# Optimization experiments

Hardware: AMD Instinct MI355X
Metric: run time of the kernel (lower is better)

The kernel has to match this reference:

```python
import jax, jax.numpy as jnp
import numpy as np


def _conv1x1(x, w, b):
    # x: [B,C,H,W], w: [O,C], b: [O] -> [B,O,H,W]
    return jnp.einsum('bchw,oc->bohw', x, w) + b[None, :, None, None]


def _maxpool2x2(x):
    # MaxPool2d(kernel_size=2, stride=2), VALID padding
    return jax.lax.reduce_window(
        x, -jnp.inf, jax.lax.max,
        window_dimensions=(1, 1, 2, 2),
        window_strides=(1, 1, 2, 2),
        padding='VALID')


def setup_inputs() -> dict:
    key = jax.random.key(0)
    ks = jax.random.split(key, 9)
    B, C, H, W = 8, 256, 64, 64
    c = 128  # in_channels // channel_scale_factor
    s = 0.05
    return {
        'x': jax.random.normal(ks[0], (B, C, H, W), jnp.float32),
        'theta_w': jax.random.normal(ks[1], (c, C), jnp.float32) * s,
        'theta_b': jax.random.normal(ks[2], (c,), jnp.float32) * s,
        'phi_w': jax.random.normal(ks[3], (c, C), jnp.float32) * s,
        'phi_b': jax.random.normal(ks[4], (c,), jnp.float32) * s,
        'g_w': jax.random.normal(ks[5], (c, C), jnp.float32) * s,
        'g_b': jax.random.normal(ks[6], (c,), jnp.float32) * s,
        'wz_w': jax.random.normal(ks[7], (C, c), jnp.float32) * s,
        'wz_b': jax.random.normal(ks[8], (C,), jnp.float32) * s,
    }


def reference(x, theta_w, theta_b, phi_w, phi_b, g_w, g_b, wz_w, wz_b):
    B, C, H, W = x.shape
    c = theta_w.shape[0]
    ox = x
    theta = _conv1x1(x, theta_w, theta_b)              # [B,c,H,W]
    xp = _maxpool2x2(x)                                # [B,C,h,w]
    phi = _conv1x1(xp, phi_w, phi_b)                   # [B,c,h,w]
    gi = _conv1x1(xp, g_w, g_b)                        # [B,c,h,w]

    N = H * W
    M = phi.shape[2] * phi.shape[3]
    theta1 = theta.reshape(B, c, N).transpose(0, 2, 1)  # [B,N,c]
    phi1 = phi.reshape(B, c, M)                         # [B,c,M]
    gi1 = gi.reshape(B, c, M).transpose(0, 2, 1)        # [B,M,c]

    m1 = jnp.einsum('bnc,bcm->bnm', theta1, phi1)       # [B,N,M] attention scores
    m1 = jax.nn.softmax(m1, axis=2)
    m2 = jnp.einsum('bnm,bmc->bnc', m1, gi1)            # [B,N,c]
    # Faithful to torch .view: raw-buffer reinterpretation, no transpose
    m3 = m2.reshape(B, c, H, W)
    m4 = _conv1x1(m3, wz_w, wz_b)                       # [B,C,H,W]
    return m4 + ox
```

## Files before the change

### kernel.cpp

```cpp
#include <hip/hip_runtime.h>
#include <math.h>

#define BATCH 8
#define CINCH 256
#define CMID  128
#define NPIX  4096
#define MPIX  1024

typedef __attribute__((ext_vector_type(8))) short bf16x8;
typedef __attribute__((ext_vector_type(4))) short s16x4;
typedef __attribute__((ext_vector_type(4))) float f32x4;

static __device__ __forceinline__ short f2bf(float f) {
    unsigned u = __float_as_uint(f);
    u = (u + 0x7fffu + ((u >> 16) & 1u)) >> 16;
    return (short)u;
}
static __device__ __forceinline__ float bf2f(short s) {
    return __uint_as_float(((unsigned)(unsigned short)s) << 16);
}

static __device__ __forceinline__ void gl16(const void* g, void* l) {
    __builtin_amdgcn_global_load_lds(
        (const __attribute__((address_space(1))) void*)g,
        (__attribute__((address_space(3))) void*)l, 16, 0, 0);
}

__global__ __launch_bounds__(256)
void wcvt_k(const float* __restrict__ a, const float* __restrict__ b,
            const float* __restrict__ c, const float* __restrict__ d,
            short* __restrict__ o)
{
    int i = (blockIdx.x * 256 + threadIdx.x) * 4;
    if (i < 32768) {
        int cr = i >> 8, col = i & 255;
        int R = (cr & 7) * 16 + (cr >> 3);
        float4 v = *(const float4*)(a + i);
        s16x4 rv = { f2bf(v.x * 1.44269504f), f2bf(v.y * 1.44269504f),
                     f2bf(v.z * 1.44269504f), f2bf(v.w * 1.44269504f) };
        *(s16x4*)(o + R * 256 + col) = rv;
    } else {
        const float* src; int j;
        if (i < 65536)      { src = b; j = i - 32768; }
        else if (i < 98304) { src = c; j = i - 65536; }
        else                { src = d; j = i - 98304; }
        float4 v = *(const float4*)(src + j);
        s16x4 rv = { f2bf(v.x), f2bf(v.y), f2bf(v.z), f2bf(v.w) };
        *(s16x4*)(o + i) = rv;
    }
}

__global__ __launch_bounds__(512)
void front_k(const float* __restrict__ x,
             const short* __restrict__ th_wh, const float* __restrict__ th_b,
             const short* __restrict__ ph_wh, const float* __restrict__ ph_b,
             const short* __restrict__ g_wh,  const float* __restrict__ g_b,
             short* __restrict__ thetaO, short* __restrict__ phiO,
             short* __restrict__ gO)
{
    __shared__ float F[128 * 65];
    __shared__ short X[128 * 264];
    __shared__ short P[32 * 264];

    const int bid = blockIdx.x;
    const int t   = threadIdx.x;
    const int b   = bid & 7;
    const int r   = bid >> 3;
    const int wv  = t >> 6;
    const int l   = t & 63;
    const int lr  = l & 15;
    const int lg  = l >> 4;

    const int hh = wv & 1;
    const int c0 = t >> 7;
    float ra[16], rb[16];
    {
        const float* xb = x + ((size_t)(b * 256)) * 4096 + r * 128;
#pragma unroll
        for (int i = 0; i < 16; ++i)
            ra[i] = xb[(size_t)(c0 + i * 4) * 4096 + hh * 64 + l];
    }
#pragma unroll
    for (int ct = 0; ct < 4; ++ct) {
        if ((ct & 1) == 0) {
#pragma unroll
            for (int i = 0; i < 16; ++i) F[(hh * 64 + l) * 65 + c0 + i * 4] = ra[i];
            if (ct < 3) {
                const float* xb = x + ((size_t)(b * 256 + (ct + 1) * 64)) * 4096 + r * 128;
#pragma unroll
                for (int i = 0; i < 16; ++i)
                    rb[i] = xb[(size_t)(c0 + i * 4) * 4096 + hh * 64 + l];
            }
        } else {
#pragma unroll
            for (int i = 0; i < 16; ++i) F[(hh * 64 + l) * 65 + c0 + i * 4] = rb[i];
            if (ct < 3) {
                const float* xb = x + ((size_t)(b * 256 + (ct + 1) * 64)) * 4096 + r * 128;
#pragma unroll
                for (int i = 0; i < 16; ++i)
                    ra[i] = xb[(size_t)(c0 + i * 4) * 4096 + hh * 64 + l];
            }
        }
        asm volatile("s_waitcnt lgkmcnt(0)" ::: "memory");
        __builtin_amdgcn_s_barrier();
#pragma unroll
        for (int i = 0; i < 16; ++i) {
            int row = wv + i * 8;
            X[row * 264 + ct * 64 + l] = f2bf(F[row * 65 + l]);
        }
        asm volatile("s_waitcnt lgkmcnt(0)" ::: "memory");
        __builtin_amdgcn_s_barrier();
    }

#pragma unroll
    for (int i = 0; i < 4; ++i) {
        int slot = i * 512 + t;
        int wp = slot >> 6, c4 = slot & 63;
        s16x4 v0 = *(const s16x4*)(X + (2 * wp) * 264 + c4 * 4);
        s16x4 v1 = *(const s16x4*)(X + (2 * wp + 1) * 264 + c4 * 4);
        s16x4 v2 = *(const s16x4*)(X + (64 + 2 * wp) * 264 + c4 * 4);
        s16x4 v3 = *(const s16x4*)(X + (65 + 2 * wp) * 264 + c4 * 4);
        s16x4 rm;
#pragma unroll
        for (int e = 0; e < 4; ++e) {
            float m = fmaxf(fmaxf(bf2f(v0[e]), bf2f(v1[e])),
                            fmaxf(bf2f(v2[e]), bf2f(v3[e])));
            rm[e] = f2bf(m);
        }
        *(s16x4*)(P + wp * 264 + c4 * 4) = rm;
    }
    __syncthreads();

    {
        const int m0 = wv * 16;
        f32x4 o[8];
#pragma unroll
        for (int dt = 0; dt < 8; ++dt)
#pragma unroll
            for (int e = 0; e < 4; ++e) o[dt][e] = 0.f;
        for (int kt = 0; kt < 8; ++kt) {
            bf16x8 a = *(const bf16x8*)(X + (m0 + lr) * 264 + kt * 32 + lg * 8);
#pragma unroll
            for (int dt = 0; dt < 8; ++dt) {
                bf16x8 bv = *(const bf16x8*)(th_wh + (size_t)(dt * 16 + lr) * 256 + kt * 32 + lg * 8);
                o[dt] = __builtin_amdgcn_mfma_f32_16x16x32_bf16(a, bv, o[dt], 0, 0, 0);
            }
        }
        float bvt[8];
#pragma unroll
        for (int dt = 0; dt < 8; ++dt) bvt[dt] = th_b[lr * 8 + dt] * 1.44269504f;
        short* ob = thetaO + (size_t)b * NPIX * 128;
#pragma unroll
        for (int rr = 0; rr < 4; ++rr) {
            int n = r * 128 + m0 + lg * 4 + rr;
            bf16x8 sv;
#pragma unroll
            for (int dt = 0; dt < 8; ++dt) sv[dt] = f2bf(o[dt][rr] + bvt[dt]);
            *(bf16x8*)(ob + (size_t)n * 128 + lr * 8) = sv;
        }
    }

    {
        const int half = wv & 1;
        const int coH  = (wv >> 1) & 1;
        const short* wsel = ((wv < 4) ? ph_wh : g_wh) + (size_t)coH * 64 * 256;
        const float* bsel = (wv < 4) ? ph_b : g_b;

        f32x4 q[4];
#pragma unroll
        for (int dt = 0; dt < 4; ++dt)
#pragma unroll
            for (int e = 0; e < 4; ++e) q[dt][e] = 0.f;
        for (int kt = 0; kt < 8; ++kt) {
            bf16x8 a = *(const bf16x8*)(P + (half * 16 + lr) * 264 + kt * 32 + lg * 8);
#pragma unroll
            for (int dt = 0; dt < 4; ++dt) {
                bf16x8 bv = *(const bf16x8*)(wsel + (size_t)(dt * 16 + lr) * 256 + kt * 32 + lg * 8);
                q[dt] = __builtin_amdgcn_mfma_f32_16x16x32_bf16(a, bv, q[dt], 0, 0, 0);
            }
        }
        float bv4[4];
#pragma unroll
        for (int dt = 0; dt < 4; ++dt) bv4[dt] = bsel[coH * 64 + dt * 16 + lr];

        if (wv < 4) {
            short* cb = phiO + (size_t)b * 32 * 4096 + (size_t)r * 4096;
#pragma unroll
            for (int rr = 0; rr < 4; ++rr) {
                int mloc = half * 16 + lg * 4 + rr;
                short* cbb = cb + (mloc >> 4) * 512 + (mloc & 15) * 8;
#pragma unroll
                for (int dt = 0; dt < 4; ++dt) {
                    int cc = coH * 64 + dt * 16 + lr;
                    cbb[(cc >> 5) * 1024 + ((cc >> 3) & 3) * 128 + (cc & 7)]
                        = f2bf(q[dt][rr] + bv4[dt]);
                }
            }
        } else {
            short* cb = gO + (size_t)b * 32 * 4096 + (size_t)r * 4096;
            const int keyblk = half * 2 + (lg >> 1);
#pragma unroll
            for (int dt = 0; dt < 4; ++dt) {
                int cc = coH * 64 + dt * 16 + lr;
                s16x4 sv;
#pragma unroll
                for (int rr = 0; rr < 4; ++rr) sv[rr] = f2bf(q[dt][rr] + bv4[dt]);
                *(s16x4*)(cb + (size_t)((cc >> 4) * 64 + keyblk * 16 + (cc & 15)) * 8
                             + (lg & 1) * 4) = sv;
            }
        }
    }
}

__global__ __launch_bounds__(512)
void attn_fz(const short* __restrict__ theta, const short* __restrict__ phi_sw,
             const short* __restrict__ G_sw, const short* __restrict__ wzh,
             const float* __restrict__ wzb, const float* __restrict__ x,
             float* __restrict__ out)
{
    __shared__ __align__(16) char smem[147456];
    const int t   = threadIdx.x;
    const int wv  = t >> 6;
    const int l   = t & 63;
    const int lr  = l & 15;
    const int lg  = l >> 4;
    const int gid = wv >> 2;
    const int wvl = wv & 3;
    const int bid = blockIdx.x;
    const int b   = bid & 7;
    const int s   = bid >> 3;

    const short* thb = theta + (size_t)b * NPIX * 128;
    const char*  phC = (const char*)phi_sw + (size_t)b * 32 * 8192;
    const char*  gC  = (const char*)G_sw  + (size_t)b * 32 * 8192;
    const int first = gid * 16;

    auto STAGEP = [&](int bufi, int pi) {
#pragma unroll
        for (int sub = 0; sub < 2; ++sub) {
            int chunk = first + pi * 2 + sub;
            const char* ps = phC + (size_t)chunk * 8192 + wvl * 2048 + l * 16;
            const char* gs = gC  + (size_t)chunk * 8192 + wvl * 2048 + l * 16;
            char* base = smem + gid * 65536 + bufi * 32768 + sub * 16384;
            gl16(ps,        base + wvl * 2048);
            gl16(ps + 1024, base + wvl * 2048 + 1024);
            gl16(gs,        base + 8192 + wvl * 2048);
            gl16(gs + 1024, base + 8192 + wvl * 2048 + 1024);
        }
    };

    STAGEP(0, 0);

    bf16x8 bq[2][4];
#pragma unroll
    for (int u = 0; u < 2; ++u) {
        int n = ((wvl * 2 + u) * 16 + lr) * 32 + s;
#pragma unroll
        for (int kt = 0; kt < 4; ++kt)
            bq[u][kt] = *(const bf16x8*)(thb + (size_t)n * 128 + kt * 32 + lg * 8);
    }

    f32x4 o[2][8];
#pragma unroll
    for (int u = 0; u < 2; ++u)
#pragma unroll
        for (int dt = 0; dt < 8; ++dt)
#pragma unroll
            for (int e = 0; e < 4; ++e) o[u][dt][e] = 0.f;
    float ps_[2] = { 0.f, 0.f };

    for (int pi = 0; pi < 8; ++pi) {
        asm volatile("s_waitcnt vmcnt(0)" ::: "memory");
        __builtin_amdgcn_s_barrier();
        if (pi < 7) STAGEP((pi + 1) & 1, pi + 1);

#pragma unroll
        for (int sub = 0; sub < 2; ++sub) {
            const short* pb = (const short*)(smem + gid * 65536 + (pi & 1) * 32768
                                             + sub * 16384);
            const short* gb = pb + 4096;

            f32x4 ssw[2][2];
#pragma unroll
            for (int u = 0; u < 2; ++u)
#pragma unroll
                for (int mt = 0; mt < 2; ++mt)
#pragma unroll
                    for (int e = 0; e < 4; ++e) ssw[u][mt][e] = 0.f;
#pragma unroll
            for (int kt = 0; kt < 4; ++kt) {
                bf16x8 a0 = *(const bf16x8*)(pb + ((kt * 2 + 0) * 64 + l) * 8);
                bf16x8 a1 = *(const bf16x8*)(pb + ((kt * 2 + 1) * 64 + l) * 8);
#pragma unroll
                for (int u = 0; u < 2; ++u) {
                    ssw[u][0] = __builtin_amdgcn_mfma_f32_16x16x32_bf16(a0, bq[u][kt], ssw[u][0], 0, 0, 0);
                    ssw[u][1] = __builtin_amdgcn_mfma_f32_16x16x32_bf16(a1, bq[u][kt], ssw[u][1], 0, 0, 0);
                }
            }

            bf16x8 gf[8];
#pragma unroll
            for (int dt = 0; dt < 8; ++dt)
                gf[dt] = *(const bf16x8*)(gb + (dt * 64 + l) * 8);

#pragma unroll
            for (int u = 0; u < 2; ++u) {
                short* pu = (short*)(smem + 131072 + wv * 2048 + u * 1024);
#pragma unroll
                for (int mt = 0; mt < 2; ++mt) {
                    s16x4 pv;
#pragma unroll
                    for (int rr = 0; rr < 4; ++rr) {
                        float p = exp2f(ssw[u][mt][rr] - 40.f);
                        ps_[u] += p;
                        pv[rr] = f2bf(p);
                    }
                    *(s16x4*)(pu + ((mt * 2 + (lg >> 1)) * 16 + lr) * 8 + (lg & 1) * 4) = pv;
                }
                bf16x8 pa = *(const bf16x8*)(pu + l * 8);
#pragma unroll
                for (int dt = 0; dt < 8; ++dt)
                    o[u][dt] = __builtin_amdgcn_mfma_f32_16x16x32_bf16(pa, gf[dt], o[u][dt], 0, 0, 0);
            }
        }
    }

    __syncthreads();
    float* mg = (float*)smem;
    short* m3l = (short*)(smem + 73728);
    if (wv >= 4) {
        float* mb = mg + (size_t)((wv - 4) * 64 + l) * 68;
#pragma unroll
        for (int u = 0; u < 2; ++u)
#pragma unroll
            for (int dt = 0; dt < 8; ++dt)
                *(f32x4*)(mb + (u * 8 + dt) * 4) = o[u][dt];
        mb[64] = ps_[0]; mb[65] = ps_[1];
    }
    __syncthreads();
    if (wv < 4) {
        const float* mb = mg + (size_t)(wv * 64 + l) * 68;
#pragma unroll
        for (int u = 0; u < 2; ++u)
#pragma unroll
            for (int dt = 0; dt < 8; ++dt) {
                f32x4 pv = *(const f32x4*)(mb + (u * 8 + dt) * 4);
#pragma unroll
                for (int e = 0; e < 4; ++e) o[u][dt][e] += pv[e];
            }
        ps_[0] += mb[64]; ps_[1] += mb[65];

#pragma unroll
        for (int u = 0; u < 2; ++u) {
            float tot = ps_[u];
            tot += __shfl_xor(tot, 16);
            tot += __shfl_xor(tot, 32);
            float inv = 1.f / tot;
            float invg[4];
#pragma unroll
            for (int rr = 0; rr < 4; ++rr) invg[rr] = __shfl(inv, lg * 4 + rr);
            const int cmb = (wvl * 2 + u) * 2 + (lg >> 1);
#pragma unroll
            for (int dt = 0; dt < 8; ++dt) {
                s16x4 zv;
#pragma unroll
                for (int rr = 0; rr < 4; ++rr) zv[rr] = f2bf(o[u][dt][rr] * invg[rr]);
                *(s16x4*)(m3l + (size_t)(cmb * 128 + dt * 16 + lr) * 8 + (lg & 1) * 4) = zv;
            }
        }
    }
    __syncthreads();

    {
        const int co0 = wv * 32;
        bf16x8 afr[2][4];
#pragma unroll
        for (int nt = 0; nt < 2; ++nt) {
            int co = co0 + nt * 16 + lr;
#pragma unroll
            for (int kt = 0; kt < 4; ++kt)
                afr[nt][kt] = *(const bf16x8*)(wzh + (size_t)co * 128 + kt * 32 + lg * 8);
        }
        f32x4 oc[2][8];
#pragma unroll
        for (int nt = 0; nt < 2; ++nt)
#pragma unroll
            for (int dt = 0; dt < 8; ++dt)
#pragma unroll
                for (int e = 0; e < 4; ++e) oc[nt][dt][e] = 0.f;

#pragma unroll
        for (int dt = 0; dt < 8; ++dt) {
#pragma unroll
            for (int kt = 0; kt < 4; ++kt) {
                bf16x8 bz = *(const bf16x8*)(m3l + (size_t)((kt * 4 + lg) * 128 + dt * 16 + lr) * 8);
                oc[0][dt] = __builtin_amdgcn_mfma_f32_16x16x32_bf16(afr[0][kt], bz, oc[0][dt], 0, 0, 0);
                oc[1][dt] = __builtin_amdgcn_mfma_f32_16x16x32_bf16(afr[1][kt], bz, oc[1][dt], 0, 0, 0);
            }
        }

#pragma unroll
        for (int nt = 0; nt < 2; ++nt)
#pragma unroll
            for (int rr = 0; rr < 4; ++rr) {
                int co = co0 + nt * 16 + lg * 4 + rr;
                float bv = wzb[co];
                const float* xb = x + ((size_t)b * 256 + co) * 4096 + s * 128;
                float* ob = out + ((size_t)b * 256 + co) * 4096 + s * 128;
#pragma unroll
                for (int dt = 0; dt < 8; ++dt) {
                    int lp = dt * 16 + lr;
                    ob[lp] = oc[nt][dt][rr] + bv + xb[lp];
                }
            }
    }
}

extern "C" void kernel_launch(void* const* d_in, const int* in_sizes, int n_in,
                              void* d_out, int out_size, void* d_ws, size_t ws_size,
                              hipStream_t stream)
{
    const float* x       = (const float*)d_in[0];
    const float* theta_w = (const float*)d_in[1];
    const float* theta_b = (const float*)d_in[2];
    const float* phi_w   = (const float*)d_in[3];
    const float* phi_b   = (const float*)d_in[4];
    const float* g_w     = (const float*)d_in[5];
    const float* g_b     = (const float*)d_in[6];
    const float* wz_w    = (const float*)d_in[7];
    const float* wz_b    = (const float*)d_in[8];
    float* out = (float*)d_out;

    short* ws      = (short*)d_ws;
    short* theta_h = ws;
    short* phi_h   = theta_h + (size_t)4194304;
    short* G_h     = phi_h + (size_t)1048576;
    short* wh      = G_h  + (size_t)1048576;
    short* th_wh = wh;
    short* ph_wh = wh + 32768;
    short* g_wh  = wh + 65536;
    short* wz_wh = wh + 98304;

    wcvt_k<<<dim3(128), 256, 0, stream>>>(theta_w, phi_w, g_w, wz_w, wh);

    front_k<<<dim3(256), 512, 0, stream>>>(x, th_wh, theta_b, ph_wh, phi_b,
                                           g_wh, g_b, theta_h, phi_h, G_h);

    attn_fz<<<dim3(256), 512, 0, stream>>>(theta_h, phi_h, G_h,
                                           wz_wh, wz_b, x, out);
}
```

Before: 73.32 us.

## Widen front kernel to 1024 threads and prefetch epilogue operands earlier

```diff
diff --git a/kernel.cpp b/kernel.cpp
--- a/kernel.cpp
+++ b/kernel.cpp
@@ -50,7 +50,7 @@
     }
 }
 
-__global__ __launch_bounds__(512)
+__global__ __launch_bounds__(1024)
 void front_k(const float* __restrict__ x,
              const short* __restrict__ th_wh, const float* __restrict__ th_b,
              const short* __restrict__ ph_wh, const float* __restrict__ ph_b,
@@ -72,49 +72,50 @@
     const int lg  = l >> 4;
 
     const int hh = wv & 1;
-    const int c0 = t >> 7;
-    float ra[16], rb[16];
+    const int c0 = wv >> 1;
+    float ra[8], rb[8];
     {
         const float* xb = x + ((size_t)(b * 256)) * 4096 + r * 128;
 #pragma unroll
-        for (int i = 0; i < 16; ++i)
-            ra[i] = xb[(size_t)(c0 + i * 4) * 4096 + hh * 64 + l];
+        for (int i = 0; i < 8; ++i)
+            ra[i] = xb[(size_t)(c0 + i * 8) * 4096 + hh * 64 + l];
     }
 #pragma unroll
     for (int ct = 0; ct < 4; ++ct) {
         if ((ct & 1) == 0) {
 #pragma unroll
-            for (int i = 0; i < 16; ++i) F[(hh * 64 + l) * 65 + c0 + i * 4] = ra[i];
+            for (int i = 0; i < 8; ++i) F[(hh * 64 + l) * 65 + c0 + i * 8] = ra[i];
             if (ct < 3) {
                 const float* xb = x + ((size_t)(b * 256 + (ct + 1) * 64)) * 4096 + r * 128;
 #pragma unroll
-                for (int i = 0; i < 16; ++i)
-                    rb[i] = xb[(size_t)(c0 + i * 4) * 4096 + hh * 64 + l];
+                for (int i = 0; i < 8; ++i)
+                    rb[i] = xb[(size_t)(c0 + i * 8) * 4096 + hh * 64 + l];
             }
         } else {
 #pragma unroll
-            for (int i = 0; i < 16; ++i) F[(hh * 64 + l) * 65 + c0 + i * 4] = rb[i];
+            for (int i = 0; i < 8; ++i) F[(hh * 64 + l) * 65 + c0 + i * 8] = rb[i];
             if (ct < 3) {
                 const float* xb = x + ((size_t)(b * 256 + (ct + 1) * 64)) * 4096 + r * 128;
 #pragma unroll
-                for (int i = 0; i < 16; ++i)
-                    ra[i] = xb[(size_t)(c0 + i * 4) * 4096 + hh * 64 + l];
+                for (int i = 0; i < 8; ++i)
+                    ra[i] = xb[(size_t)(c0 + i * 8) * 4096 + hh * 64 + l];
             }
         }
         asm volatile("s_waitcnt lgkmcnt(0)" ::: "memory");
         __builtin_amdgcn_s_barrier();
 #pragma unroll
-        for (int i = 0; i < 16; ++i) {
-            int row = wv + i * 8;
-            X[row * 264 + ct * 64 + l] = f2bf(F[row * 65 + l]);
+        for (int i = 0; i < 8; ++i) {
+            int slot = i * 1024 + t;
+            int row = slot >> 6, ch = slot & 63;
+            X[row * 264 + ct * 64 + ch] = f2bf(F[row * 65 + ch]);
         }
         asm volatile("s_waitcnt lgkmcnt(0)" ::: "memory");
         __builtin_amdgcn_s_barrier();
     }
 
 #pragma unroll
-    for (int i = 0; i < 4; ++i) {
-        int slot = i * 512 + t;
+    for (int i = 0; i < 2; ++i) {
+        int slot = i * 1024 + t;
         int wp = slot >> 6, c4 = slot & 63;
         s16x4 v0 = *(const s16x4*)(X + (2 * wp) * 264 + c4 * 4);
         s16x4 v1 = *(const s16x4*)(X + (2 * wp + 1) * 264 + c4 * 4);
@@ -131,7 +132,7 @@
     }
     __syncthreads();
 
-    {
+    if (wv < 8) {
         const int m0 = wv * 16;
         f32x4 o[8];
 #pragma unroll
@@ -158,13 +159,13 @@
             for (int dt = 0; dt < 8; ++dt) sv[dt] = f2bf(o[dt][rr] + bvt[dt]);
             *(bf16x8*)(ob + (size_t)n * 128 + lr * 8) = sv;
         }
-    }
-
-    {
-        const int half = wv & 1;
-        const int coH  = (wv >> 1) & 1;
-        const short* wsel = ((wv < 4) ? ph_wh : g_wh) + (size_t)coH * 64 * 256;
-        const float* bsel = (wv < 4) ? ph_b : g_b;
+    } else {
+        const int j    = wv & 3;
+        const int half = j & 1;
+        const int coH  = j >> 1;
+        const bool isPhi = (wv < 12);
+        const short* wsel = (isPhi ? ph_wh : g_wh) + (size_t)coH * 64 * 256;
+        const float* bsel = isPhi ? ph_b : g_b;
 
         f32x4 q[4];
 #pragma unroll
@@ -183,7 +184,7 @@
 #pragma unroll
         for (int dt = 0; dt < 4; ++dt) bv4[dt] = bsel[coH * 64 + dt * 16 + lr];
 
-        if (wv < 4) {
+        if (isPhi) {
             short* cb = phiO + (size_t)b * 32 * 4096 + (size_t)r * 4096;
 #pragma unroll
             for (int rr = 0; rr < 4; ++rr) {
@@ -325,6 +326,16 @@
         }
     }
 
+    const int co0 = wv * 32;
+    bf16x8 afr[2][4];
+#pragma unroll
+    for (int nt = 0; nt < 2; ++nt) {
+        int co = co0 + nt * 16 + lr;
+#pragma unroll
+        for (int kt = 0; kt < 4; ++kt)
+            afr[nt][kt] = *(const bf16x8*)(wzh + (size_t)co * 128 + kt * 32 + lg * 8);
+    }
+
     __syncthreads();
     float* mg = (float*)smem;
     short* m3l = (short*)(smem + 73728);
@@ -372,15 +383,18 @@
     __syncthreads();
 
     {
-        const int co0 = wv * 32;
-        bf16x8 afr[2][4];
-#pragma unroll
-        for (int nt = 0; nt < 2; ++nt) {
-            int co = co0 + nt * 16 + lr;
-#pragma unroll
-            for (int kt = 0; kt < 4; ++kt)
-                afr[nt][kt] = *(const bf16x8*)(wzh + (size_t)co * 128 + kt * 32 + lg * 8);
-        }
+        float xr[2][4][8];
+#pragma unroll
+        for (int nt = 0; nt < 2; ++nt)
+#pragma unroll
+            for (int rr = 0; rr < 4; ++rr) {
+                int co = co0 + nt * 16 + lg * 4 + rr;
+                const float* xb = x + ((size_t)b * 256 + co) * 4096 + s * 128;
+#pragma unroll
+                for (int dt = 0; dt < 8; ++dt)
+                    xr[nt][rr][dt] = xb[dt * 16 + lr];
+            }
+
         f32x4 oc[2][8];
 #pragma unroll
         for (int nt = 0; nt < 2; ++nt)
@@ -405,12 +419,11 @@
             for (int rr = 0; rr < 4; ++rr) {
                 int co = co0 + nt * 16 + lg * 4 + rr;
                 float bv = wzb[co];
-                const float* xb = x + ((size_t)b * 256 + co) * 4096 + s * 128;
                 float* ob = out + ((size_t)b * 256 + co) * 4096 + s * 128;
 #pragma unroll
                 for (int dt = 0; dt < 8; ++dt) {
                     int lp = dt * 16 + lr;
-                    ob[lp] = oc[nt][dt][rr] + bv + xb[lp];
+                    ob[lp] = oc[nt][dt][rr] + bv + xr[nt][rr][dt];
                 }
             }
     }
@@ -443,8 +456,8 @@
 
     wcvt_k<<<dim3(128), 256, 0, stream>>>(theta_w, phi_w, g_w, wz_w, wh);
 
-    front_k<<<dim3(256), 512, 0, stream>>>(x, th_wh, theta_b, ph_wh, phi_b,
-                                           g_wh, g_b, theta_h, phi_h, G_h);
+    front_k<<<dim3(256), 1024, 0, stream>>>(x, th_wh, theta_b, ph_wh, phi_b,
+                                            g_wh, g_b, theta_h, phi_h, G_h);
 
     attn_fz<<<dim3(256), 512, 0, stream>>>(theta_h, phi_h, G_h,
                                            wz_wh, wz_b, x, out);
```

After: 74.48 us. No clear change (+1.6%).

## Drop LDS staging and split-key reduction; stream phi/G directly from global

Applied to the files above, without the earlier changes.

```diff
diff --git a/kernel.cpp b/kernel.cpp
--- a/kernel.cpp
+++ b/kernel.cpp
@@ -18,12 +18,6 @@
 }
 static __device__ __forceinline__ float bf2f(short s) {
     return __uint_as_float(((unsigned)(unsigned short)s) << 16);
-}
-
-static __device__ __forceinline__ void gl16(const void* g, void* l) {
-    __builtin_amdgcn_global_load_lds(
-        (const __attribute__((address_space(1))) void*)g,
-        (__attribute__((address_space(3))) void*)l, 16, 0, 0);
 }
 
 __global__ __launch_bounds__(256)
@@ -212,49 +206,30 @@
     }
 }
 
-__global__ __launch_bounds__(512)
+__global__ __launch_bounds__(256, 2)
 void attn_fz(const short* __restrict__ theta, const short* __restrict__ phi_sw,
              const short* __restrict__ G_sw, const short* __restrict__ wzh,
              const float* __restrict__ wzb, const float* __restrict__ x,
              float* __restrict__ out)
 {
-    __shared__ __align__(16) char smem[147456];
+    __shared__ __align__(16) char smem[36864];
     const int t   = threadIdx.x;
     const int wv  = t >> 6;
     const int l   = t & 63;
     const int lr  = l & 15;
     const int lg  = l >> 4;
-    const int gid = wv >> 2;
-    const int wvl = wv & 3;
     const int bid = blockIdx.x;
     const int b   = bid & 7;
     const int s   = bid >> 3;
 
     const short* thb = theta + (size_t)b * NPIX * 128;
-    const char*  phC = (const char*)phi_sw + (size_t)b * 32 * 8192;
-    const char*  gC  = (const char*)G_sw  + (size_t)b * 32 * 8192;
-    const int first = gid * 16;
-
-    auto STAGEP = [&](int bufi, int pi) {
-#pragma unroll
-        for (int sub = 0; sub < 2; ++sub) {
-            int chunk = first + pi * 2 + sub;
-            const char* ps = phC + (size_t)chunk * 8192 + wvl * 2048 + l * 16;
-            const char* gs = gC  + (size_t)chunk * 8192 + wvl * 2048 + l * 16;
-            char* base = smem + gid * 65536 + bufi * 32768 + sub * 16384;
-            gl16(ps,        base + wvl * 2048);
-            gl16(ps + 1024, base + wvl * 2048 + 1024);
-            gl16(gs,        base + 8192 + wvl * 2048);
-            gl16(gs + 1024, base + 8192 + wvl * 2048 + 1024);
-        }
-    };
-
-    STAGEP(0, 0);
+    const short* phC = phi_sw + (size_t)b * 32 * 4096;
+    const short* gC  = G_sw  + (size_t)b * 32 * 4096;
 
     bf16x8 bq[2][4];
 #pragma unroll
     for (int u = 0; u < 2; ++u) {
-        int n = ((wvl * 2 + u) * 16 + lr) * 32 + s;
+        int n = ((wv * 2 + u) * 16 + lr) * 32 + s;
 #pragma unroll
         for (int kt = 0; kt < 4; ++kt)
             bq[u][kt] = *(const bf16x8*)(thb + (size_t)n * 128 + kt * 32 + lg * 8);
@@ -269,150 +244,122 @@
             for (int e = 0; e < 4; ++e) o[u][dt][e] = 0.f;
     float ps_[2] = { 0.f, 0.f };
 
-    for (int pi = 0; pi < 8; ++pi) {
-        asm volatile("s_waitcnt vmcnt(0)" ::: "memory");
-        __builtin_amdgcn_s_barrier();
-        if (pi < 7) STAGEP((pi + 1) & 1, pi + 1);
-
-#pragma unroll
-        for (int sub = 0; sub < 2; ++sub) {
-            const short* pb = (const short*)(smem + gid * 65536 + (pi & 1) * 32768
-                                             + sub * 16384);
-            const short* gb = pb + 4096;
-
-            f32x4 ssw[2][2];
-#pragma unroll
-            for (int u = 0; u < 2; ++u)
-#pragma unroll
-                for (int mt = 0; mt < 2; ++mt)
-#pragma unroll
-                    for (int e = 0; e < 4; ++e) ssw[u][mt][e] = 0.f;
-#pragma unroll
-            for (int kt = 0; kt < 4; ++kt) {
-                bf16x8 a0 = *(const bf16x8*)(pb + ((kt * 2 + 0) * 64 + l) * 8);
-                bf16x8 a1 = *(const bf16x8*)(pb + ((kt * 2 + 1) * 64 + l) * 8);
-#pragma unroll
-                for (int u = 0; u < 2; ++u) {
-                    ssw[u][0] = __builtin_amdgcn_mfma_f32_16x16x32_bf16(a0, bq[u][kt], ssw[u][0], 0, 0, 0);
-                    ssw[u][1] = __builtin_amdgcn_mfma_f32_16x16x32_bf16(a1, bq[u][kt], ssw[u][1], 0, 0, 0);
+    short* pu = (short*)(smem + 32768) + wv * 512;
+
+    for (int c = 0; c < 32; ++c) {
+        const short* pc = phC + (size_t)c * 4096;
+        const short* gc = gC  + (size_t)c * 4096;
+
+        bf16x8 af[8];
+#pragma unroll
+        for (int i = 0; i < 8; ++i)
+            af[i] = *(const bf16x8*)(pc + (i * 64 + l) * 8);
+        bf16x8 gf[8];
+#pragma unroll
+        for (int dt = 0; dt < 8; ++dt)
+            gf[dt] = *(const bf16x8*)(gc + (dt * 64 + l) * 8);
+
+        f32x4 ssw[2][2];
+#pragma unroll
+        for (int u = 0; u < 2; ++u)
+#pragma unroll
+            for (int mt = 0; mt < 2; ++mt)
+#pragma unroll
+                for (int e = 0; e < 4; ++e) ssw[u][mt][e] = 0.f;
+#pragma unroll
+        for (int kt = 0; kt < 4; ++kt) {
+#pragma unroll
+            for (int u = 0; u < 2; ++u) {
+                ssw[u][0] = __builtin_amdgcn_mfma_f32_16x16x32_bf16(af[kt * 2 + 0], bq[u][kt], ssw[u][0], 0, 0, 0);
+                ssw[u][1] = __builtin_amdgcn_mfma_f32_16x16x32_bf16(af[kt * 2 + 1], bq[u][kt], ssw[u][1], 0, 0, 0);
+            }
+        }
+
+#pragma unroll
+        for (int u = 0; u < 2; ++u) {
+#pragma unroll
+            for (int mt = 0; mt < 2; ++mt) {
+                s16x4 pv;
+#pragma unroll
+                for (int rr = 0; rr < 4; ++rr) {
+                    float p = exp2f(ssw[u][mt][rr] - 40.f);
+                    ps_[u] += p;
+                    pv[rr] = f2bf(p);
                 }
-            }
-
-            bf16x8 gf[8];
+                *(s16x4*)(pu + ((mt * 2 + (lg >> 1)) * 16 + lr) * 8 + (lg & 1) * 4) = pv;
+            }
+            bf16x8 pa = *(const bf16x8*)(pu + l * 8);
 #pragma unroll
             for (int dt = 0; dt < 8; ++dt)
-                gf[dt] = *(const bf16x8*)(gb + (dt * 64 + l) * 8);
-
-#pragma unroll
-            for (int u = 0; u < 2; ++u) {
-                short* pu = (short*)(smem + 131072 + wv * 2048 + u * 1024);
-#pragma unroll
-                for (int mt = 0; mt < 2; ++mt) {
-                    s16x4 pv;
-#pragma unroll
-                    for (int rr = 0; rr < 4; ++rr) {
-                        float p = exp2f(ssw[u][mt][rr] - 40.f);
-                        ps_[u] += p;
-                        pv[rr] = f2bf(p);
-                    }
-                    *(s16x4*)(pu + ((mt * 2 + (lg >> 1)) * 16 + lr) * 8 + (lg & 1) * 4) = pv;
-                }
-                bf16x8 pa = *(const bf16x8*)(pu + l * 8);
-#pragma unroll
-                for (int dt = 0; dt < 8; ++dt)
-                    o[u][dt] = __builtin_amdgcn_mfma_f32_16x16x32_bf16(pa, gf[dt], o[u][dt], 0, 0, 0);
-            }
-        }
-    }
-
+                o[u][dt] = __builtin_amdgcn_mfma_f32_16x16x32_bf16(pa, gf[dt], o[u][dt], 0, 0, 0);
+        }
+    }
+
+    short* m3l = (short*)smem;
+#pragma unroll
+    for (int u = 0; u < 2; ++u) {
+        float tot = ps_[u];
+        tot += __shfl_xor(tot, 16);
+        tot += __shfl_xor(tot, 32);
+        float inv = 1.f / tot;
+        float invg[4];
+#pragma unroll
+        for (int rr = 0; rr < 4; ++rr) invg[rr] = __shfl(inv, lg * 4 + rr);
+        const int cmb = (wv * 2 + u) * 2 + (lg >> 1);
+#pragma unroll
+        for (int dt = 0; dt < 8; ++dt) {
+            s16x4 zv;
+#pragma unroll
+            for (int rr = 0; rr < 4; ++rr) zv[rr] = f2bf(o[u][dt][rr] * invg[rr]);
+            *(s16x4*)(m3l + (size_t)(cmb * 128 + dt * 16 + lr) * 8 + (lg & 1) * 4) = zv;
+        }
+    }
     __syncthreads();
-    float* mg = (float*)smem;
-    short* m3l = (short*)(smem + 73728);
-    if (wv >= 4) {
-        float* mb = mg + (size_t)((wv - 4) * 64 + l) * 68;
-#pragma unroll
-        for (int u = 0; u < 2; ++u)
+
+#pragma unroll
+    for (int nt = 0; nt < 4; ++nt) {
+        const int co0 = wv * 64 + nt * 16;
+        bf16x8 afr[4];
+#pragma unroll
+        for (int kt = 0; kt < 4; ++kt)
+            afr[kt] = *(const bf16x8*)(wzh + (size_t)(co0 + lr) * 128 + kt * 32 + lg * 8);
+
+        float xr[4][8];
+#pragma unroll
+        for (int rr = 0; rr < 4; ++rr) {
+            int co = co0 + lg * 4 + rr;
+            const float* xb = x + ((size_t)b * 256 + co) * 4096 + s * 128;
 #pragma unroll
             for (int dt = 0; dt < 8; ++dt)
-                *(f32x4*)(mb + (u * 8 + dt) * 4) = o[u][dt];
-        mb[64] = ps_[0]; mb[65] = ps_[1];
-    }
-    __syncthreads();
-    if (wv < 4) {
-        const float* mb = mg + (size_t)(wv * 64 + l) * 68;
-#pragma unroll
-        for (int u = 0; u < 2; ++u)
-#pragma unroll
-            for (int dt = 0; dt < 8; ++dt) {
-                f32x4 pv = *(const f32x4*)(mb + (u * 8 + dt) * 4);
-#pragma unroll
-                for (int e = 0; e < 4; ++e) o[u][dt][e] += pv[e];
-            }
-        ps_[0] += mb[64]; ps_[1] += mb[65];
-
-#pragma unroll
-        for (int u = 0; u < 2; ++u) {
-            float tot = ps_[u];
-            tot += __shfl_xor(tot, 16);
-            tot += __shfl_xor(tot, 32);
-            float inv = 1.f / tot;
-            float invg[4];
-#pragma unroll
-            for (int rr = 0; rr < 4; ++rr) invg[rr] = __shfl(inv, lg * 4 + rr);
-            const int cmb = (wvl * 2 + u) * 2 + (lg >> 1);
-#pragma unroll
-            for (int dt = 0; dt < 8; ++dt) {
-                s16x4 zv;
-#pragma unroll
-                for (int rr = 0; rr < 4; ++rr) zv[rr] = f2bf(o[u][dt][rr] * invg[rr]);
-                *(s16x4*)(m3l + (size_t)(cmb * 128 + dt * 16 + lr) * 8 + (lg & 1) * 4) = zv;
-            }
-        }
-    }
-    __syncthreads();
-
-    {
-        const int co0 = wv * 32;
-        bf16x8 afr[2][4];
-#pragma unroll
-        for (int nt = 0; nt < 2; ++nt) {
-            int co = co0 + nt * 16 + lr;
-#pragma unroll
-            for (int kt = 0; kt < 4; ++kt)
-                afr[nt][kt] = *(const bf16x8*)(wzh + (size_t)co * 128 + kt * 32 + lg * 8);
-        }
-        f32x4 oc[2][8];
-#pragma unroll
-        for (int nt = 0; nt < 2; ++nt)
-#pragma unroll
-            for (int dt = 0; dt < 8; ++dt)
-#pragma unroll
-                for (int e = 0; e < 4; ++e) oc[nt][dt][e] = 0.f;
+                xr[rr][dt] = xb[dt * 16 + lr];
+        }
+
+        f32x4 oc[8];
+#pragma unroll
+        for (int dt = 0; dt < 8; ++dt)
+#pragma unroll
+            for (int e = 0; e < 4; ++e) oc[dt][e] = 0.f;
 
 #pragma unroll
         for (int dt = 0; dt < 8; ++dt) {
 #pragma unroll
             for (int kt = 0; kt < 4; ++kt) {
                 bf16x8 bz = *(const bf16x8*)(m3l + (size_t)((kt * 4 + lg) * 128 + dt * 16 + lr) * 8);
-                oc[0][dt] = __builtin_amdgcn_mfma_f32_16x16x32_bf16(afr[0][kt], bz, oc[0][dt], 0, 0, 0);
-                oc[1][dt] = __builtin_amdgcn_mfma_f32_16x16x32_bf16(afr[1][kt], bz, oc[1][dt], 0, 0, 0);
-            }
-        }
-
-#pragma unroll
-        for (int nt = 0; nt < 2; ++nt)
-#pragma unroll
-            for (int rr = 0; rr < 4; ++rr) {
-                int co = co0 + nt * 16 + lg * 4 + rr;
-                float bv = wzb[co];
-                const float* xb = x + ((size_t)b * 256 + co) * 4096 + s * 128;
-                float* ob = out + ((size_t)b * 256 + co) * 4096 + s * 128;
-#pragma unroll
-                for (int dt = 0; dt < 8; ++dt) {
-                    int lp = dt * 16 + lr;
-                    ob[lp] = oc[nt][dt][rr] + bv + xb[lp];
-                }
-            }
+                oc[dt] = __builtin_amdgcn_mfma_f32_16x16x32_bf16(afr[kt], bz, oc[dt], 0, 0, 0);
+            }
+        }
+
+#pragma unroll
+        for (int rr = 0; rr < 4; ++rr) {
+            int co = co0 + lg * 4 + rr;
+            float bv = wzb[co];
+            float* ob = out + ((size_t)b * 256 + co) * 4096 + s * 128;
+#pragma unroll
+            for (int dt = 0; dt < 8; ++dt) {
+                int lp = dt * 16 + lr;
+                ob[lp] = oc[dt][rr] + bv + xr[rr][dt];
+            }
+        }
     }
 }
 
@@ -446,6 +393,6 @@
     front_k<<<dim3(256), 512, 0, stream>>>(x, th_wh, theta_b, ph_wh, phi_b,
                                            g_wh, g_b, theta_h, phi_h, G_h);
 
-    attn_fz<<<dim3(256), 512, 0, stream>>>(theta_h, phi_h, G_h,
+    attn_fz<<<dim3(256), 256, 0, stream>>>(theta_h, phi_h, G_h,
                                            wz_wh, wz_b, x, out);
 }
```

Measured after the change: 95.25 us. 29.9% more time.
